# Optimization experiments

Hardware: AMD Instinct MI355X
Metric: run time of the kernel (lower is better)

## Reference

```python
import jax, jax.numpy as jnp
import numpy as np

B, T, D, V = 64, 2048, 64, 100000


def create_beta_stack(feats, times):
    """feats: [F,B,T] float, times: [B,T] float.
    beta[:, :, i] = (times[:,i]-times[:,i-1] + mask_{i-1} * beta[:,:,i-1]) * (times[:,i] != -1)
    where mask = (feat != -1) & (feat != 0). Sequential reset/accumulate scan over T."""
    dt = times[:, 1:] - times[:, :-1]                                   # [B, T-1]
    mask = ((feats[:, :, :-1] != -1) & (feats[:, :, :-1] != 0)).astype(feats.dtype)  # [F,B,T-1]
    pad = (times[:, 1:] != -1).astype(feats.dtype)                      # [B, T-1]

    def step(b, xs):
        dt_i, m_i, p_i = xs                      # [B], [F,B], [B]
        b_new = (dt_i[None, :] + m_i * b) * p_i[None, :]
        return b_new, b_new

    init = jnp.zeros(feats.shape[:2], feats.dtype)                      # [F,B]
    _, betas = jax.lax.scan(step, init, (dt.T, jnp.moveaxis(mask, 2, 0), pad.T))  # [T-1,F,B]
    beta = jnp.concatenate([init[None], betas], axis=0)                 # [T,F,B]
    return jnp.moveaxis(beta, 0, 2)                                     # [F,B,T]


def setup_inputs() -> dict:
    key = jax.random.key(0)
    ks = jax.random.split(key, 11)
    cat1 = jax.random.randint(ks[0], (B, T), 0, V)
    cat2 = jax.random.randint(ks[1], (B, T), 0, V)
    num1 = jax.random.normal(ks[2], (B, T), jnp.float32)
    num2 = jax.random.normal(ks[3], (B, T), jnp.float32)
    # integer-valued, sorted per row (event timestamps); no -1 padding
    event_time = jnp.sort(jax.random.randint(ks[4], (B, T), 0, 10000), axis=1).astype(jnp.float32)
    E1 = jax.random.normal(ks[5], (V, D), jnp.float32) * 0.02
    E2 = jax.random.normal(ks[6], (V, D), jnp.float32) * 0.02
    w1 = jax.random.normal(ks[7], (D,), jnp.float32) * 0.02
    b1 = jax.random.normal(ks[8], (D,), jnp.float32) * 0.02
    w2 = jax.random.normal(ks[9], (D,), jnp.float32) * 0.02
    b2 = jax.random.normal(ks[10], (D,), jnp.float32) * 0.02
    return {"cat1": cat1, "cat2": cat2, "num1": num1, "num2": num2,
            "event_time": event_time, "E1": E1, "E2": E2,
            "w1": w1, "b1": b1, "w2": w2, "b2": b2}


def reference(cat1, cat2, num1, num2, event_time, E1, E2, w1, b1, w2, b2):
    times = event_time.astype(jnp.float32)
    # categorical embeddings [B,T,D]
    emb1 = E1[cat1]
    emb2 = E2[cat2]
    # numeric Linear(1, D): values[...,None] @ W.T + b
    nemb1 = num1[..., None] * w1 + b1
    nemb2 = num2[..., None] * w2 + b2
    # time-since-last-valid-event recurrence, stacked over all 4 features
    feats = jnp.stack([cat1.astype(jnp.float32), cat2.astype(jnp.float32), num1, num2], axis=0)  # [4,B,T]
    betas = create_beta_stack(feats, times)                             # [4,B,T]
    rep = lambda x: jnp.broadcast_to(x[..., None], x.shape + (D,))
    delta = jnp.concatenate([rep(betas[0]), rep(betas[1]), rep(betas[2]), rep(betas[3])], axis=-1)  # [B,T,4D]
    m = lambda v: rep((v != -1) & (v != 0))
    mask = jnp.concatenate([m(cat1), m(cat2), m(num1), m(num2)], axis=-1)  # [B,T,4D] bool
    features = jnp.concatenate([emb1, emb2, nemb1, nemb2], axis=-1)     # [B,T,4D]
    return (features, times, delta, mask)
```

## Files before the change

### kernel.cpp

```cpp
#include <hip/hip_runtime.h>

#define BB 64
#define TT 2048
#define DD 64
#define BT (BB * TT)
#define OFF_F 0
#define OFF_T (BT * 256)
#define OFF_D (OFF_T + BT)
#define OFF_M (OFF_D + BT * 256)

typedef float v4f __attribute__((ext_vector_type(4)));

__device__ __forceinline__ void nt_store4(float* p, float x, float y, float z, float w) {
    v4f v = {x, y, z, w};
    __builtin_nontemporal_store(v, (v4f*)p);
}
__device__ __forceinline__ void nt_store4v(float* p, float4 v) {
    nt_store4(p, v.x, v.y, v.z, v.w);
}

__global__ __launch_bounds__(64) void beta_scan_kernel(
    const int* __restrict__ cat1, const int* __restrict__ cat2,
    const float* __restrict__ num1, const float* __restrict__ num2,
    const float* __restrict__ times, float* __restrict__ beta_ws)
{
    const int f    = blockIdx.x >> 6;
    const int b    = blockIdx.x & 63;
    const int lane = threadIdx.x;
    const int lo   = lane * 32;

    const float* trow = times + b * TT;

    float t[32], v[32];
    {
        const float4* t4 = (const float4*)(trow + lo);
        #pragma unroll
        for (int q = 0; q < 8; ++q) {
            float4 x = t4[q];
            t[4*q+0] = x.x; t[4*q+1] = x.y; t[4*q+2] = x.z; t[4*q+3] = x.w;
        }
    }
    if (f < 2) {
        const int* crow = (f == 0 ? cat1 : cat2) + b * TT;
        const int4* c4 = (const int4*)(crow + lo);
        #pragma unroll
        for (int q = 0; q < 8; ++q) {
            int4 x = c4[q];
            v[4*q+0] = (float)x.x; v[4*q+1] = (float)x.y;
            v[4*q+2] = (float)x.z; v[4*q+3] = (float)x.w;
        }
    } else {
        const float* nrow = (f == 2 ? num1 : num2) + b * TT;
        const float4* n4 = (const float4*)(nrow + lo);
        #pragma unroll
        for (int q = 0; q < 8; ++q) {
            float4 x = n4[q];
            v[4*q+0] = x.x; v[4*q+1] = x.y; v[4*q+2] = x.z; v[4*q+3] = x.w;
        }
    }
    float tprev = 0.f, vprev = 0.f;
    if (lane > 0) {
        tprev = trow[lo - 1];
        if      (f == 0) vprev = (float)cat1[b * TT + lo - 1];
        else if (f == 1) vprev = (float)cat2[b * TT + lo - 1];
        else if (f == 2) vprev = num1[b * TT + lo - 1];
        else             vprev = num2[b * TT + lo - 1];
    }

    float A = 1.f, C = 0.f;
    #pragma unroll
    for (int k = 0; k < 32; ++k) {
        float a, c;
        if (lo + k == 0) { a = 0.f; c = 0.f; }
        else {
            float ti  = t[k];
            float tp  = (k == 0) ? tprev : t[k-1];
            float fv  = (k == 0) ? vprev : v[k-1];
            float pad = (ti != -1.f) ? 1.f : 0.f;
            float m   = (fv != -1.f && fv != 0.f) ? 1.f : 0.f;
            a = m * pad;
            c = (ti - tp) * pad;
        }
        C = a * C + c;
        A = A * a;
    }
    for (int d = 1; d < 64; d <<= 1) {
        float Ap = __shfl_up(A, d);
        float Cp = __shfl_up(C, d);
        if (lane >= d) { C = A * Cp + C; A = A * Ap; }
    }
    float beta = __shfl_up(C, 1);
    if (lane == 0) beta = 0.f;

    float* out = beta_ws + (size_t)b * TT * 4 + f;
    #pragma unroll
    for (int k = 0; k < 32; ++k) {
        float a, c;
        if (lo + k == 0) { a = 0.f; c = 0.f; }
        else {
            float ti  = t[k];
            float tp  = (k == 0) ? tprev : t[k-1];
            float fv  = (k == 0) ? vprev : v[k-1];
            float pad = (ti != -1.f) ? 1.f : 0.f;
            float m   = (fv != -1.f && fv != 0.f) ? 1.f : 0.f;
            a = m * pad;
            c = (ti - tp) * pad;
        }
        beta = a * beta + c;
        out[(lo + k) * 4] = beta;
    }
}

__global__ __launch_bounds__(256, 8) void expand_kernel(
    const int* __restrict__ cat1, const int* __restrict__ cat2,
    const float* __restrict__ num1, const float* __restrict__ num2,
    const float* __restrict__ times,
    const float* __restrict__ E1, const float* __restrict__ E2,
    const float* __restrict__ w1, const float* __restrict__ b1,
    const float* __restrict__ w2, const float* __restrict__ b2,
    const float* __restrict__ beta_ws, float* __restrict__ out)
{
    const int u  = blockIdx.x * 256 + threadIdx.x;
    const int bt = u >> 4;
    const int c  = u & 15;

    const int   i1 = cat1[bt];
    const int   i2 = cat2[bt];
    const float x1 = num1[bt];
    const float x2 = num2[bt];

    const float4 e1  = ((const float4*)(E1 + (size_t)i1 * DD))[c];
    const float4 e2  = ((const float4*)(E2 + (size_t)i2 * DD))[c];
    const float4 wc1 = ((const float4*)w1)[c];
    const float4 bc1 = ((const float4*)b1)[c];
    const float4 wc2 = ((const float4*)w2)[c];
    const float4 bc2 = ((const float4*)b2)[c];
    const float4 n1  = make_float4(x1 * wc1.x + bc1.x, x1 * wc1.y + bc1.y,
                                   x1 * wc1.z + bc1.z, x1 * wc1.w + bc1.w);
    const float4 n2  = make_float4(x2 * wc2.x + bc2.x, x2 * wc2.y + bc2.y,
                                   x2 * wc2.z + bc2.z, x2 * wc2.w + bc2.w);

    const float4 bet = ((const float4*)beta_ws)[bt];

    const float m1 = (i1 != -1 && i1 != 0) ? 1.f : 0.f;
    const float m2 = (i2 != -1 && i2 != 0) ? 1.f : 0.f;
    const float m3 = (x1 != -1.f && x1 != 0.f) ? 1.f : 0.f;
    const float m4 = (x2 != -1.f && x2 != 0.f) ? 1.f : 0.f;

    const int base = bt * 64 + c;
    float* outF = out + OFF_F;
    float* outD = out + OFF_D;
    float* outM = out + OFF_M;

    nt_store4v(outF + 4 * (base),      e1);
    nt_store4v(outF + 4 * (base + 16), e2);
    nt_store4v(outF + 4 * (base + 32), n1);
    nt_store4v(outF + 4 * (base + 48), n2);

    nt_store4(outD + 4 * (base),      bet.x, bet.x, bet.x, bet.x);
    nt_store4(outD + 4 * (base + 16), bet.y, bet.y, bet.y, bet.y);
    nt_store4(outD + 4 * (base + 32), bet.z, bet.z, bet.z, bet.z);
    nt_store4(outD + 4 * (base + 48), bet.w, bet.w, bet.w, bet.w);

    nt_store4(outM + 4 * (base),      m1, m1, m1, m1);
    nt_store4(outM + 4 * (base + 16), m2, m2, m2, m2);
    nt_store4(outM + 4 * (base + 32), m3, m3, m3, m3);
    nt_store4(outM + 4 * (base + 48), m4, m4, m4, m4);

    if (u < BT / 4) {
        float4 t = ((const float4*)times)[u];
        nt_store4v(out + OFF_T + 4 * u, t);
    }
}

extern "C" void kernel_launch(void* const* d_in, const int* in_sizes, int n_in,
                              void* d_out, int out_size, void* d_ws, size_t ws_size,
                              hipStream_t stream) {
    const int*   cat1  = (const int*)d_in[0];
    const int*   cat2  = (const int*)d_in[1];
    const float* num1  = (const float*)d_in[2];
    const float* num2  = (const float*)d_in[3];
    const float* times = (const float*)d_in[4];
    const float* E1    = (const float*)d_in[5];
    const float* E2    = (const float*)d_in[6];
    const float* w1    = (const float*)d_in[7];
    const float* b1    = (const float*)d_in[8];
    const float* w2    = (const float*)d_in[9];
    const float* b2    = (const float*)d_in[10];
    float* out     = (float*)d_out;
    float* beta_ws = (float*)d_ws;

    beta_scan_kernel<<<4 * BB, 64, 0, stream>>>(cat1, cat2, num1, num2, times, beta_ws);

    expand_kernel<<<(BT * 16) / 256, 256, 0, stream>>>(
        cat1, cat2, num1, num2, times, E1, E2, w1, b1, w2, b2, beta_ws, out);
}
```

Before: 458.4 us.

## Map one wavefront per (b,t) row so each thread stores one contiguous float4

The expand kernel now gives each wavefront a single (b,t) position, and each lane writes one float4 per output tensor. Before, each thread wrote four strided float4s per tensor. Consecutive lanes now cover one contiguous 1 KB segment per output, which should make the streaming nontemporal stores fully coalesced. The cost is four times as many threads, with the per-row index, beta and mask loads repeated across lanes, plus per-lane selects. The occupancy hint in launch_bounds is dropped.

Measured after the change: 451.6 us. No clear change (-1.5%).

```diff
diff --git a/kernel.cpp b/kernel.cpp
--- a/kernel.cpp
+++ b/kernel.cpp
@@ -111,7 +111,7 @@
     }
 }
 
-__global__ __launch_bounds__(256, 8) void expand_kernel(
+__global__ __launch_bounds__(256) void expand_kernel(
     const int* __restrict__ cat1, const int* __restrict__ cat2,
     const float* __restrict__ num1, const float* __restrict__ num2,
     const float* __restrict__ times,
@@ -120,52 +120,47 @@
     const float* __restrict__ w2, const float* __restrict__ b2,
     const float* __restrict__ beta_ws, float* __restrict__ out)
 {
-    const int u  = blockIdx.x * 256 + threadIdx.x;
-    const int bt = u >> 4;
-    const int c  = u & 15;
+    const int u    = blockIdx.x * 256 + threadIdx.x;
+    const int lane = threadIdx.x & 63;
+    const int wid  = __builtin_amdgcn_readfirstlane((int)(threadIdx.x >> 6));
+    const int bt   = (blockIdx.x << 2) | wid;
+    const int q    = lane >> 4;
+    const int c    = lane & 15;
 
     const int   i1 = cat1[bt];
     const int   i2 = cat2[bt];
     const float x1 = num1[bt];
     const float x2 = num2[bt];
-
-    const float4 e1  = ((const float4*)(E1 + (size_t)i1 * DD))[c];
-    const float4 e2  = ((const float4*)(E2 + (size_t)i2 * DD))[c];
-    const float4 wc1 = ((const float4*)w1)[c];
-    const float4 bc1 = ((const float4*)b1)[c];
-    const float4 wc2 = ((const float4*)w2)[c];
-    const float4 bc2 = ((const float4*)b2)[c];
-    const float4 n1  = make_float4(x1 * wc1.x + bc1.x, x1 * wc1.y + bc1.y,
-                                   x1 * wc1.z + bc1.z, x1 * wc1.w + bc1.w);
-    const float4 n2  = make_float4(x2 * wc2.x + bc2.x, x2 * wc2.y + bc2.y,
-                                   x2 * wc2.z + bc2.z, x2 * wc2.w + bc2.w);
-
     const float4 bet = ((const float4*)beta_ws)[bt];
 
-    const float m1 = (i1 != -1 && i1 != 0) ? 1.f : 0.f;
-    const float m2 = (i2 != -1 && i2 != 0) ? 1.f : 0.f;
+    const float* srcA = (q == 0) ? E1 + (size_t)i1 * DD
+                      : (q == 1) ? E2 + (size_t)i2 * DD
+                      : (q == 2) ? w1 : w2;
+    const float* srcB = (q == 3) ? b2 : b1;
+    const float  x    = (q == 3) ? x2 : x1;
+
+    const float4 a  = ((const float4*)srcA)[c];
+    const float4 bb = ((const float4*)srcB)[c];
+
+    float4 nv = make_float4(fmaf(x, a.x, bb.x), fmaf(x, a.y, bb.y),
+                            fmaf(x, a.z, bb.z), fmaf(x, a.w, bb.w));
+    float4 val;
+    val.x = (q < 2) ? a.x : nv.x;
+    val.y = (q < 2) ? a.y : nv.y;
+    val.z = (q < 2) ? a.z : nv.z;
+    val.w = (q < 2) ? a.w : nv.w;
+
+    const float m1 = (i1 != -1   && i1 != 0  ) ? 1.f : 0.f;
+    const float m2 = (i2 != -1   && i2 != 0  ) ? 1.f : 0.f;
     const float m3 = (x1 != -1.f && x1 != 0.f) ? 1.f : 0.f;
     const float m4 = (x2 != -1.f && x2 != 0.f) ? 1.f : 0.f;
+    const float m  = (q == 0) ? m1 : (q == 1) ? m2 : (q == 2) ? m3 : m4;
+    const float bv = (q == 0) ? bet.x : (q == 1) ? bet.y : (q == 2) ? bet.z : bet.w;
 
-    const int base = bt * 64 + c;
-    float* outF = out + OFF_F;
-    float* outD = out + OFF_D;
-    float* outM = out + OFF_M;
-
-    nt_store4v(outF + 4 * (base),      e1);
-    nt_store4v(outF + 4 * (base + 16), e2);
-    nt_store4v(outF + 4 * (base + 32), n1);
-    nt_store4v(outF + 4 * (base + 48), n2);
-
-    nt_store4(outD + 4 * (base),      bet.x, bet.x, bet.x, bet.x);
-    nt_store4(outD + 4 * (base + 16), bet.y, bet.y, bet.y, bet.y);
-    nt_store4(outD + 4 * (base + 32), bet.z, bet.z, bet.z, bet.z);
-    nt_store4(outD + 4 * (base + 48), bet.w, bet.w, bet.w, bet.w);
-
-    nt_store4(outM + 4 * (base),      m1, m1, m1, m1);
-    nt_store4(outM + 4 * (base + 16), m2, m2, m2, m2);
-    nt_store4(outM + 4 * (base + 32), m3, m3, m3, m3);
-    nt_store4(outM + 4 * (base + 48), m4, m4, m4, m4);
+    const size_t o = ((size_t)bt << 6) | (size_t)lane;
+    nt_store4v(out + OFF_F + (o << 2), val);
+    nt_store4 (out + OFF_D + (o << 2), bv, bv, bv, bv);
+    nt_store4 (out + OFF_M + (o << 2), m, m, m, m);
 
     if (u < BT / 4) {
         float4 t = ((const float4*)times)[u];
@@ -192,6 +187,6 @@
 
     beta_scan_kernel<<<4 * BB, 64, 0, stream>>>(cat1, cat2, num1, num2, times, beta_ws);
 
-    expand_kernel<<<(BT * 16) / 256, 256, 0, stream>>>(
+    expand_kernel<<<(BT * 64) / 256, 256, 0, stream>>>(
         cat1, cat2, num1, num2, times, E1, E2, w1, b1, w2, b2, beta_ws, out);
 }
```
